# Optimization experiments

Measured on AMD Instinct MI355X. Metric: run time of the kernel, lower is better.

The kernel has to match this reference:

```python
import jax, jax.numpy as jnp
import numpy as np

Q, S, D = 8192, 30, 512
THRESH = 30


def setup_inputs() -> dict:
    key = jax.random.key(0)
    ks = jax.random.split(key, 8)
    return {
        "query_encode": jax.random.normal(ks[0], (Q, D), jnp.float32),
        "support_encode": jax.random.normal(ks[1], (S, D), jnp.float32),
        # binary CTR-style labels in {0,1}
        "support_y": jnp.round(jax.random.uniform(ks[2], (1, S), jnp.float32)),
        "support_predict": jax.random.normal(ks[3], (S,), jnp.float32),
        "query_predict": jax.random.normal(ks[4], (Q,), jnp.float32),
        "fc1_w": jax.random.normal(ks[5], (D,), jnp.float32) / np.sqrt(D),
        "fc1_b": jnp.zeros((), jnp.float32),
        # AdjustLayer params: scale init 6, bias init 0, shape [THRESH, 1]
        "adjust_scale": jnp.full((THRESH, 1), 6.0, jnp.float32),
        "adjust_bias": jnp.zeros((THRESH, 1), jnp.float32),
        "num_samples": S,
    }


def reference(query_encode, support_encode, support_y, support_predict,
              query_predict, fc1_w, fc1_b, adjust_scale, adjust_bias,
              num_samples):
    # Pairwise L1 distance: [Q, S, D]
    distance = jnp.abs(query_encode[:, None, :] - support_encode[None, :, :])
    # Linear scorer over feature dim -> [Q, S]
    similar_score = jnp.einsum("qsd,d->qs", distance, fc1_w) + fc1_b
    attn = jax.nn.softmax(similar_score, axis=1)  # softmax over support dim
    # Residual of support labels vs predictor output: [1, S]
    delta_y = support_y - jax.nn.sigmoid(support_predict)[None, :]
    delta_y_hat = jnp.sum(delta_y * attn, axis=1)  # [Q]
    # AdjustLayer: indexed scale/bias (index is a static int here)
    scale = jnp.abs(adjust_scale[num_samples - 1, 0])
    bias = adjust_bias[num_samples - 1, 0]
    prediction = delta_y_hat * scale + bias + query_predict  # [Q]
    # Mean L2 distance to support set: [Q]
    mean_l2 = jnp.mean(jnp.sqrt(jnp.sum(distance ** 2, axis=-1)), axis=-1)
    return prediction, mean_l2
```

## Files before the change

### kernel.cpp

```cpp
#include <hip/hip_runtime.h>
#include <math.h>


#define QN 8192
#define SN 30
#define DN 512
#define BLK 512
#define QT 16
#define SCHUNK 10
#define NPASS 3
#define SROW 580
#define PRW 17
#define PSTR 31

__global__ __launch_bounds__(BLK, 2)
void resus_one(const float* __restrict__ query,
               const float* __restrict__ support,
               const float* __restrict__ support_y,
               const float* __restrict__ support_pr,
               const float* __restrict__ query_pr,
               const float* __restrict__ fc1_w,
               const float* __restrict__ adj_scale,
               const float* __restrict__ adj_bias,
               const int*   __restrict__ num_samples,
               float* __restrict__ out)
{
    __shared__ float  sp[SCHUNK * SROW];
    __shared__ float  praw_sc[SCHUNK * QT * PRW];
    __shared__ float  praw_sq[SCHUNK * QT * PRW];
    __shared__ float2 part[QT * PSTR];

    const int tid   = threadIdx.x;
    const int ql    = tid & 15;
    const int dseg  = (tid >> 4) & 15;
    const int shalf = tid >> 8;
    const int q     = blockIdx.x * QT + ql;
    const bool has2 = (tid < 256);

#define SCAT(V, I) { const int i_ = (I), row_ = i_ >> 7, c4_ = i_ & 127; \
    *reinterpret_cast<float4*>(sp + row_ * SROW + 36 * (c4_ >> 3) + 4 * (c4_ & 7)) = (V); }

    {
        const float4* sg0 = reinterpret_cast<const float4*>(support);
        float4 g0 = sg0[tid];
        float4 g1 = sg0[tid + 512];
        float4 g2;
        if (has2) g2 = sg0[tid + 1024];
        SCAT(g0, tid)
        SCAT(g1, tid + 512)
        if (has2) SCAT(g2, tid + 1024)
    }
    __syncthreads();
    asm volatile("" ::: "memory");

    const float* qp = query + (size_t)q * DN + dseg * 32;
    const float* wp = fc1_w + dseg * 32;
    float4 a0 = *reinterpret_cast<const float4*>(qp +  0);
    float4 w0 = *reinterpret_cast<const float4*>(wp +  0);
    float4 a1 = *reinterpret_cast<const float4*>(qp +  4);
    float4 w1 = *reinterpret_cast<const float4*>(wp +  4);
    float4 a2 = *reinterpret_cast<const float4*>(qp +  8);
    float4 w2 = *reinterpret_cast<const float4*>(wp +  8);
    float4 a3 = *reinterpret_cast<const float4*>(qp + 12);
    float4 w3 = *reinterpret_cast<const float4*>(wp + 12);
    float4 a4 = *reinterpret_cast<const float4*>(qp + 16);
    float4 w4 = *reinterpret_cast<const float4*>(wp + 16);
    float4 a5 = *reinterpret_cast<const float4*>(qp + 20);
    float4 w5 = *reinterpret_cast<const float4*>(wp + 20);
    float4 a6 = *reinterpret_cast<const float4*>(qp + 24);
    float4 w6 = *reinterpret_cast<const float4*>(wp + 24);
    float4 a7 = *reinterpret_cast<const float4*>(qp + 28);
    float4 w7 = *reinterpret_cast<const float4*>(wp + 28);

    const float4* sg1 = reinterpret_cast<const float4*>(support + (size_t)SCHUNK * DN);
    float4 h0 = sg1[tid];
    float4 h1 = sg1[tid + 512];
    float4 h2;
    if (has2) h2 = sg1[tid + 1024];

#define ACCD(QV, WV, SV, SC, SQ) { float d_; \
    d_ = (QV).x - (SV).x; SC = fmaf((WV).x, fabsf(d_), SC); SQ = fmaf(d_, d_, SQ); \
    d_ = (QV).y - (SV).y; SC = fmaf((WV).y, fabsf(d_), SC); SQ = fmaf(d_, d_, SQ); \
    d_ = (QV).z - (SV).z; SC = fmaf((WV).z, fabsf(d_), SC); SQ = fmaf(d_, d_, SQ); \
    d_ = (QV).w - (SV).w; SC = fmaf((WV).w, fabsf(d_), SC); SQ = fmaf(d_, d_, SQ); }

    const int sbase = dseg * 36;
    const int pbase = ql * PRW + dseg;
    const int sl0   = shalf * (SCHUNK / 2);

    {
        const float* r0 = sp + (sl0 + 0) * SROW + sbase;
        const float* r1 = sp + (sl0 + 1) * SROW + sbase;
        const float* r2 = sp + (sl0 + 2) * SROW + sbase;
        const float* r3 = sp + (sl0 + 3) * SROW + sbase;
        const float* r4 = sp + (sl0 + 4) * SROW + sbase;
        float sc0 = 0.0f, sc1 = 0.0f, sc2 = 0.0f, sc3 = 0.0f, sc4 = 0.0f;
        float sq0 = 0.0f, sq1 = 0.0f, sq2 = 0.0f, sq3 = 0.0f, sq4 = 0.0f;

#define SEG0(AJ, WJ, OFF) { float4 s_; \
    s_ = *reinterpret_cast<const float4*>(r0 + (OFF)); ACCD(AJ, WJ, s_, sc0, sq0); \
    s_ = *reinterpret_cast<const float4*>(r1 + (OFF)); ACCD(AJ, WJ, s_, sc1, sq1); \
    s_ = *reinterpret_cast<const float4*>(r2 + (OFF)); ACCD(AJ, WJ, s_, sc2, sq2); \
    s_ = *reinterpret_cast<const float4*>(r3 + (OFF)); ACCD(AJ, WJ, s_, sc3, sq3); \
    s_ = *reinterpret_cast<const float4*>(r4 + (OFF)); ACCD(AJ, WJ, s_, sc4, sq4); }

        SEG0(a0, w0,  0) SEG0(a1, w1,  4) SEG0(a2, w2,  8) SEG0(a3, w3, 12)
        SEG0(a4, w4, 16) SEG0(a5, w5, 20) SEG0(a6, w6, 24) SEG0(a7, w7, 28)
#undef SEG0

        praw_sc[(sl0 + 0) * (QT * PRW) + pbase] = sc0;
        praw_sq[(sl0 + 0) * (QT * PRW) + pbase] = sq0;
        praw_sc[(sl0 + 1) * (QT * PRW) + pbase] = sc1;
        praw_sq[(sl0 + 1) * (QT * PRW) + pbase] = sq1;
        praw_sc[(sl0 + 2) * (QT * PRW) + pbase] = sc2;
        praw_sq[(sl0 + 2) * (QT * PRW) + pbase] = sq2;
        praw_sc[(sl0 + 3) * (QT * PRW) + pbase] = sc3;
        praw_sq[(sl0 + 3) * (QT * PRW) + pbase] = sq3;
        praw_sc[(sl0 + 4) * (QT * PRW) + pbase] = sc4;
        praw_sq[(sl0 + 4) * (QT * PRW) + pbase] = sq4;
    }

#define PIN4(V) asm volatile("" : "+v"((V).x), "+v"((V).y), "+v"((V).z), "+v"((V).w))
    PIN4(a0); PIN4(a1); PIN4(a2); PIN4(a3);
    PIN4(a4); PIN4(a5); PIN4(a6); PIN4(a7);
    PIN4(w0); PIN4(w1); PIN4(w2); PIN4(w3);
    PIN4(w4); PIN4(w5); PIN4(w6); PIN4(w7);
#undef PIN4

    __syncthreads();

    SCAT(h0, tid)
    SCAT(h1, tid + 512)
    if (has2) SCAT(h2, tid + 1024)

    if (tid < SCHUNK * QT) {
        const int sl = tid >> 4, qq = tid & 15;
        const int b = sl * (QT * PRW) + qq * PRW;
        float sc = 0.0f, sq = 0.0f;
#pragma unroll
        for (int d = 0; d < 16; ++d) {
            sc += praw_sc[b + d];
            sq += praw_sq[b + d];
        }
        part[qq * PSTR + sl] = make_float2(sc, sq);
    }
    __syncthreads();
    asm volatile("" ::: "memory");

    const float4* sg2 = reinterpret_cast<const float4*>(support + (size_t)2 * SCHUNK * DN);
    float4 k0 = sg2[tid];
    float4 k1 = sg2[tid + 512];
    float4 k2;
    if (has2) k2 = sg2[tid + 1024];

#define ACC4(QV, WV, SV) { float d_; \
    d_ = (QV).x - (SV).x; sc = fmaf((WV).x, fabsf(d_), sc); sq = fmaf(d_, d_, sq); \
    d_ = (QV).y - (SV).y; sc = fmaf((WV).y, fabsf(d_), sc); sq = fmaf(d_, d_, sq); \
    d_ = (QV).z - (SV).z; sc = fmaf((WV).z, fabsf(d_), sc); sq = fmaf(d_, d_, sq); \
    d_ = (QV).w - (SV).w; sc = fmaf((WV).w, fabsf(d_), sc); sq = fmaf(d_, d_, sq); }

#define HOTPASS \
    _Pragma("unroll") \
    for (int k = 0; k < SCHUNK / 2; ++k) { \
        const int sl = sl0 + k; \
        const float* sr = sp + sl * SROW + sbase; \
        const float4 s0 = *reinterpret_cast<const float4*>(sr +  0); \
        const float4 s1 = *reinterpret_cast<const float4*>(sr +  4); \
        const float4 s2 = *reinterpret_cast<const float4*>(sr +  8); \
        const float4 s3 = *reinterpret_cast<const float4*>(sr + 12); \
        const float4 s4 = *reinterpret_cast<const float4*>(sr + 16); \
        const float4 s5 = *reinterpret_cast<const float4*>(sr + 20); \
        const float4 s6 = *reinterpret_cast<const float4*>(sr + 24); \
        const float4 s7 = *reinterpret_cast<const float4*>(sr + 28); \
        float sc = 0.0f, sq = 0.0f; \
        ACC4(a0, w0, s0) ACC4(a1, w1, s1) \
        ACC4(a2, w2, s2) ACC4(a3, w3, s3) \
        ACC4(a4, w4, s4) ACC4(a5, w5, s5) \
        ACC4(a6, w6, s6) ACC4(a7, w7, s7) \
        praw_sc[sl * (QT * PRW) + pbase] = sc; \
        praw_sq[sl * (QT * PRW) + pbase] = sq; \
    }

    HOTPASS
    __syncthreads();

    SCAT(k0, tid)
    SCAT(k1, tid + 512)
    if (has2) SCAT(k2, tid + 1024)

    if (tid < SCHUNK * QT) {
        const int sl = tid >> 4, qq = tid & 15;
        const int b = sl * (QT * PRW) + qq * PRW;
        float sc = 0.0f, sq = 0.0f;
#pragma unroll
        for (int d = 0; d < 16; ++d) {
            sc += praw_sc[b + d];
            sq += praw_sq[b + d];
        }
        part[qq * PSTR + SCHUNK + sl] = make_float2(sc, sq);
    }
    __syncthreads();

    HOTPASS
    __syncthreads();

    if (tid < SCHUNK * QT) {
        const int sl = tid >> 4, qq = tid & 15;
        const int b = sl * (QT * PRW) + qq * PRW;
        float sc = 0.0f, sq = 0.0f;
#pragma unroll
        for (int d = 0; d < 16; ++d) {
            sc += praw_sc[b + d];
            sq += praw_sq[b + d];
        }
        part[qq * PSTR + 2 * SCHUNK + sl] = make_float2(sc, sq);
    }
#undef HOTPASS
#undef ACC4
#undef ACCD
#undef SCAT
    __syncthreads();

    const int grp  = tid >> 5;
    const int s32  = tid & 31;
    const bool valid = (s32 < SN);
    const int  si  = valid ? s32 : 0;

    float dy = 0.0f;
    if (valid)
        dy = support_y[s32] - 1.0f / (1.0f + expf(-support_pr[s32]));

    const int ns = num_samples[0];
    const float ascale = fabsf(adj_scale[ns - 1]);
    const float abias  = adj_bias[ns - 1];

    const int qg = blockIdx.x * QT + grp;
    const float2 pr = part[grp * PSTR + si];

    float scv = valid ? pr.x : -1e30f;
    float ssv = valid ? pr.y : 0.0f;

    float m = scv;
#pragma unroll
    for (int off = 16; off >= 1; off >>= 1)
        m = fmaxf(m, __shfl_xor(m, off));

    float e   = valid ? expf(scv - m) : 0.0f;
    float den = e;
    float num = dy * e;
    float l2  = valid ? sqrtf(ssv) : 0.0f;
#pragma unroll
    for (int off = 16; off >= 1; off >>= 1) {
        den += __shfl_xor(den, off);
        num += __shfl_xor(num, off);
        l2  += __shfl_xor(l2,  off);
    }

    if (s32 == 0) {
        out[qg]      = num / den * ascale + abias + query_pr[qg];
        out[QN + qg] = l2 * (1.0f / (float)SN);
    }
}

extern "C" void kernel_launch(void* const* d_in, const int* in_sizes, int n_in,
                              void* d_out, int out_size, void* d_ws, size_t ws_size,
                              hipStream_t stream)
{
    const float* query      = (const float*)d_in[0];
    const float* support    = (const float*)d_in[1];
    const float* support_y  = (const float*)d_in[2];
    const float* support_pr = (const float*)d_in[3];
    const float* query_pr   = (const float*)d_in[4];
    const float* fc1_w      = (const float*)d_in[5];
    const float* adj_scale  = (const float*)d_in[7];
    const float* adj_bias   = (const float*)d_in[8];
    const int*   num_s      = (const int*)d_in[9];
    float* out = (float*)d_out;

    dim3 grid(QN / QT);
    hipLaunchKernelGGL(resus_one, grid, dim3(BLK), 0, stream,
                       query, support, support_y, support_pr, query_pr,
                       fc1_w, adj_scale, adj_bias, num_s, out);
}
```

Baseline: 98.41 us.

## Double-buffer support chunks and split reduce/staging across thread groups

Support chunks now go into two shared-memory buffers instead of one. The global loads for the next chunk are no longer prefetched into registers by all threads. Instead, threads 192-511 load and scatter the next chunk while threads 0-159 do the partial reduction in the same phase. This frees registers and changes the barrier pattern, but the global loads are no longer overlapped with the hot compute pass, and shared memory grows by about 23KB, which may reduce occupancy.

Measured after the change: 93.39 us. 5.1% less time.

```diff
diff --git a/kernel.cpp b/kernel.cpp
--- a/kernel.cpp
+++ b/kernel.cpp
@@ -25,7 +25,7 @@
                const int*   __restrict__ num_samples,
                float* __restrict__ out)
 {
-    __shared__ float  sp[SCHUNK * SROW];
+    __shared__ float  sp[2][SCHUNK * SROW];
     __shared__ float  praw_sc[SCHUNK * QT * PRW];
     __shared__ float  praw_sq[SCHUNK * QT * PRW];
     __shared__ float2 part[QT * PSTR];
@@ -37,8 +37,8 @@
     const int q     = blockIdx.x * QT + ql;
     const bool has2 = (tid < 256);
 
-#define SCAT(V, I) { const int i_ = (I), row_ = i_ >> 7, c4_ = i_ & 127; \
-    *reinterpret_cast<float4*>(sp + row_ * SROW + 36 * (c4_ >> 3) + 4 * (c4_ & 7)) = (V); }
+#define SCAT(BUF, V, I) { const int i_ = (I), row_ = i_ >> 7, c4_ = i_ & 127; \
+    *reinterpret_cast<float4*>((BUF) + row_ * SROW + 36 * (c4_ >> 3) + 4 * (c4_ & 7)) = (V); }
 
     {
         const float4* sg0 = reinterpret_cast<const float4*>(support);
@@ -46,9 +46,9 @@
         float4 g1 = sg0[tid + 512];
         float4 g2;
         if (has2) g2 = sg0[tid + 1024];
-        SCAT(g0, tid)
-        SCAT(g1, tid + 512)
-        if (has2) SCAT(g2, tid + 1024)
+        SCAT(sp[0], g0, tid)
+        SCAT(sp[0], g1, tid + 512)
+        if (has2) SCAT(sp[0], g2, tid + 1024)
     }
     __syncthreads();
     asm volatile("" ::: "memory");
@@ -72,12 +72,6 @@
     float4 a7 = *reinterpret_cast<const float4*>(qp + 28);
     float4 w7 = *reinterpret_cast<const float4*>(wp + 28);
 
-    const float4* sg1 = reinterpret_cast<const float4*>(support + (size_t)SCHUNK * DN);
-    float4 h0 = sg1[tid];
-    float4 h1 = sg1[tid + 512];
-    float4 h2;
-    if (has2) h2 = sg1[tid + 1024];
-
 #define ACCD(QV, WV, SV, SC, SQ) { float d_; \
     d_ = (QV).x - (SV).x; SC = fmaf((WV).x, fabsf(d_), SC); SQ = fmaf(d_, d_, SQ); \
     d_ = (QV).y - (SV).y; SC = fmaf((WV).y, fabsf(d_), SC); SQ = fmaf(d_, d_, SQ); \
@@ -89,11 +83,11 @@
     const int sl0   = shalf * (SCHUNK / 2);
 
     {
-        const float* r0 = sp + (sl0 + 0) * SROW + sbase;
-        const float* r1 = sp + (sl0 + 1) * SROW + sbase;
-        const float* r2 = sp + (sl0 + 2) * SROW + sbase;
-        const float* r3 = sp + (sl0 + 3) * SROW + sbase;
-        const float* r4 = sp + (sl0 + 4) * SROW + sbase;
+        const float* r0 = sp[0] + (sl0 + 0) * SROW + sbase;
+        const float* r1 = sp[0] + (sl0 + 1) * SROW + sbase;
+        const float* r2 = sp[0] + (sl0 + 2) * SROW + sbase;
+        const float* r3 = sp[0] + (sl0 + 3) * SROW + sbase;
+        const float* r4 = sp[0] + (sl0 + 4) * SROW + sbase;
         float sc0 = 0.0f, sc1 = 0.0f, sc2 = 0.0f, sc3 = 0.0f, sc4 = 0.0f;
         float sq0 = 0.0f, sq1 = 0.0f, sq2 = 0.0f, sq3 = 0.0f, sq4 = 0.0f;
 
@@ -127,31 +121,38 @@
     PIN4(w4); PIN4(w5); PIN4(w6); PIN4(w7);
 #undef PIN4
 
-    __syncthreads();
-
-    SCAT(h0, tid)
-    SCAT(h1, tid + 512)
-    if (has2) SCAT(h2, tid + 1024)
+#define REDUCE(POFF) \
+    { const int sl_ = tid >> 4, qq_ = tid & 15; \
+      const int b_ = sl_ * (QT * PRW) + qq_ * PRW; \
+      float sc_ = 0.0f, sq_ = 0.0f; \
+      _Pragma("unroll") \
+      for (int d = 0; d < 16; ++d) { \
+          sc_ += praw_sc[b_ + d]; \
+          sq_ += praw_sq[b_ + d]; \
+      } \
+      part[qq_ * PSTR + (POFF) + sl_] = make_float2(sc_, sq_); }
+
+#define STAGEF(BUF, CH) \
+    { const float4* sg_ = reinterpret_cast<const float4*>( \
+          support + (size_t)(CH) * SCHUNK * DN); \
+      const int j_ = tid - 192; \
+      float4 g0_ = sg_[j_]; \
+      float4 g1_ = sg_[j_ + 320]; \
+      float4 g2_ = sg_[j_ + 640]; \
+      float4 g3_ = sg_[j_ + 960]; \
+      SCAT(BUF, g0_, j_) \
+      SCAT(BUF, g1_, j_ + 320) \
+      SCAT(BUF, g2_, j_ + 640) \
+      SCAT(BUF, g3_, j_ + 960) }
+
+    __syncthreads();
 
     if (tid < SCHUNK * QT) {
-        const int sl = tid >> 4, qq = tid & 15;
-        const int b = sl * (QT * PRW) + qq * PRW;
-        float sc = 0.0f, sq = 0.0f;
-#pragma unroll
-        for (int d = 0; d < 16; ++d) {
-            sc += praw_sc[b + d];
-            sq += praw_sq[b + d];
-        }
-        part[qq * PSTR + sl] = make_float2(sc, sq);
-    }
-    __syncthreads();
-    asm volatile("" ::: "memory");
-
-    const float4* sg2 = reinterpret_cast<const float4*>(support + (size_t)2 * SCHUNK * DN);
-    float4 k0 = sg2[tid];
-    float4 k1 = sg2[tid + 512];
-    float4 k2;
-    if (has2) k2 = sg2[tid + 1024];
+        REDUCE(0)
+    } else if (tid >= 192) {
+        STAGEF(sp[1], 1)
+    }
+    __syncthreads();
 
 #define ACC4(QV, WV, SV) { float d_; \
     d_ = (QV).x - (SV).x; sc = fmaf((WV).x, fabsf(d_), sc); sq = fmaf(d_, d_, sq); \
@@ -159,11 +160,11 @@
     d_ = (QV).z - (SV).z; sc = fmaf((WV).z, fabsf(d_), sc); sq = fmaf(d_, d_, sq); \
     d_ = (QV).w - (SV).w; sc = fmaf((WV).w, fabsf(d_), sc); sq = fmaf(d_, d_, sq); }
 
-#define HOTPASS \
+#define HOTPASS(BUF) \
     _Pragma("unroll") \
     for (int k = 0; k < SCHUNK / 2; ++k) { \
         const int sl = sl0 + k; \
-        const float* sr = sp + sl * SROW + sbase; \
+        const float* sr = (BUF) + sl * SROW + sbase; \
         const float4 s0 = *reinterpret_cast<const float4*>(sr +  0); \
         const float4 s1 = *reinterpret_cast<const float4*>(sr +  4); \
         const float4 s2 = *reinterpret_cast<const float4*>(sr +  8); \
@@ -181,42 +182,26 @@
         praw_sq[sl * (QT * PRW) + pbase] = sq; \
     }
 
-    HOTPASS
-    __syncthreads();
-
-    SCAT(k0, tid)
-    SCAT(k1, tid + 512)
-    if (has2) SCAT(k2, tid + 1024)
+    HOTPASS(sp[1])
+    __syncthreads();
 
     if (tid < SCHUNK * QT) {
-        const int sl = tid >> 4, qq = tid & 15;
-        const int b = sl * (QT * PRW) + qq * PRW;
-        float sc = 0.0f, sq = 0.0f;
-#pragma unroll
-        for (int d = 0; d < 16; ++d) {
-            sc += praw_sc[b + d];
-            sq += praw_sq[b + d];
-        }
-        part[qq * PSTR + SCHUNK + sl] = make_float2(sc, sq);
-    }
-    __syncthreads();
-
-    HOTPASS
+        REDUCE(SCHUNK)
+    } else if (tid >= 192) {
+        STAGEF(sp[0], 2)
+    }
+    __syncthreads();
+
+    HOTPASS(sp[0])
     __syncthreads();
 
     if (tid < SCHUNK * QT) {
-        const int sl = tid >> 4, qq = tid & 15;
-        const int b = sl * (QT * PRW) + qq * PRW;
-        float sc = 0.0f, sq = 0.0f;
-#pragma unroll
-        for (int d = 0; d < 16; ++d) {
-            sc += praw_sc[b + d];
-            sq += praw_sq[b + d];
-        }
-        part[qq * PSTR + 2 * SCHUNK + sl] = make_float2(sc, sq);
+        REDUCE(2 * SCHUNK)
     }
 #undef HOTPASS
 #undef ACC4
+#undef STAGEF
+#undef REDUCE
 #undef ACCD
 #undef SCAT
     __syncthreads();
```
